# Performance work log

Measured on AMD Instinct MI355X. Metric: run time of the kernel, lower is better.

Reference implementation:

```python
import jax, jax.numpy as jnp
import numpy as np

L = 2; B = 16; H = 56; W = 56; N = H * W; D = 256
HEADS = 8; HD = 32; INNER = HEADS * HD
WIN = 7; WIN2 = WIN * WIN; NWH = H // WIN; NWW = W // WIN; NW = NWH * NWW
DISP = WIN // 2; FF = 4 * D; CPB = 512; EPS = 1e-5


def _shift_masks():
    d = DISP
    ul = np.zeros((WIN2, WIN2), np.float32)
    ul[-d * WIN:, :-d * WIN] = -np.inf
    ul[:-d * WIN, -d * WIN:] = -np.inf
    lr = np.zeros((WIN, WIN, WIN, WIN), np.float32)
    lr[:, -d:, :, :-d] = -np.inf
    lr[:, :-d, :, -d:] = -np.inf
    return jnp.asarray(ul), jnp.asarray(lr.reshape(WIN2, WIN2))

MASK_UL, MASK_LR = _shift_masks()

_idx = np.array([[i, j] for i in range(WIN) for j in range(WIN)], np.float32)
_rel = _idx[None, :, :] - _idx[:, None, :]  # (49,49,2) relative distances
REL = jnp.asarray((np.sign(_rel) * np.log1p(np.abs(_rel))).reshape(WIN2 * WIN2, 2))


def _ln(x, g, b):
    m = x.mean(-1, keepdims=True)
    v = ((x - m) ** 2).mean(-1, keepdims=True)
    return (x - m) / jnp.sqrt(v + EPS) * g + b


def _l2norm(t):
    return t / jnp.maximum(jnp.linalg.norm(t, axis=-1, keepdims=True), 1e-12)


def _window_attn(xm, qkv_w, tau, cw1, cb1, cw2, cb2, ow, ob, shifted):
    if shifted:
        xm = jnp.roll(xm, (-DISP, -DISP), (1, 2))
    qkv = xm @ qkv_w  # (B,H,W,3*INNER), no bias
    q, k, v = jnp.split(qkv, 3, axis=-1)

    def towin(t):  # (B,H,W,INNER) -> (B,heads,nw,win2,hd)
        t = t.reshape(B, NWH, WIN, NWW, WIN, HEADS, HD)
        return t.transpose(0, 5, 1, 3, 2, 4, 6).reshape(B, HEADS, NW, WIN2, HD)

    q, k, v = towin(q), towin(k), towin(v)
    # cosine-similarity attention
    dots = jnp.einsum('bhwid,bhwjd->bhwij', _l2norm(q), _l2norm(k))
    dots = dots / jnp.clip(tau, 0.01, None)[None, :, None, None, None]
    # continuous position bias MLP: 2 -> CPB -> heads
    cpb = (jax.nn.relu(REL @ cw1 + cb1) @ cw2 + cb2).reshape(WIN2, WIN2, HEADS)
    dots = dots + cpb.transpose(2, 0, 1)[None, :, None]
    if shifted:
        dots = dots.at[:, :, -NWW:].add(MASK_UL)
        dots = dots.at[:, :, NWW - 1::NWW].add(MASK_LR)
    attn = jax.nn.softmax(dots, -1)
    out = jnp.einsum('bhwij,bhwjd->bhwid', attn, v)
    out = out.reshape(B, HEADS, NWH, NWW, WIN, WIN, HD)
    out = out.transpose(0, 2, 4, 3, 5, 1, 6).reshape(B, H, W, INNER)
    out = out @ ow + ob
    if shifted:
        out = jnp.roll(out, (DISP, DISP), (1, 2))
    return out


def _forward(x, spe, qkv_w, tau, cw1, cb1, cw2, cb2, ow, ob, ln1_g, ln1_b,
             fw1, fb1, fw2, fb2, ln2_g, ln2_b, norm_g, norm_b):
    xm = (x + spe).reshape(B, H, W, D)
    for i in range(L):
        shifted = (i % 2 == 1)
        a = _window_attn(xm, qkv_w[i], tau[i], cw1[i], cb1[i], cw2[i], cb2[i],
                         ow[i], ob[i], shifted)
        xm = _ln(a, ln1_g[i], ln1_b[i]) + xm  # Residual(PostNorm(attn))
        f = jax.nn.gelu(xm @ fw1[i] + fb1[i], approximate=False) @ fw2[i] + fb2[i]
        xm = _ln(f, ln2_g[i], ln2_b[i]) + xm  # Residual(PostNorm(mlp))
    return _ln(xm, norm_g, norm_b).reshape(B, N, D)


def setup_inputs():
    key = jax.random.key(0)
    ks = jax.random.split(key, 10)
    rn = lambda k, shp, s: jax.random.normal(k, shp, jnp.float32) * s
    return {
        'x': rn(ks[0], (B, N, D), 1.0),
        'spatial_position_embedding': rn(ks[1], (B, N, D), 0.02),
        'qkv_w': rn(ks[2], (L, D, 3 * INNER), 0.02),
        'tau': jnp.ones((L, HEADS), jnp.float32),
        'cw1': rn(ks[3], (L, 2, CPB), 0.1),
        'cb1': jnp.zeros((L, CPB), jnp.float32),
        'cw2': rn(ks[4], (L, CPB, HEADS), 0.05),
        'cb2': jnp.zeros((L, HEADS), jnp.float32),
        'ow': rn(ks[5], (L, INNER, D), 0.02),
        'ob': jnp.zeros((L, D), jnp.float32),
        'ln1_g': jnp.ones((L, D), jnp.float32),
        'ln1_b': jnp.zeros((L, D), jnp.float32),
        'fw1': rn(ks[6], (L, D, FF), 0.02),
        'fb1': jnp.zeros((L, FF), jnp.float32),
        'fw2': rn(ks[7], (L, FF, D), 0.02),
        'fb2': jnp.zeros((L, D), jnp.float32),
        'ln2_g': jnp.ones((L, D), jnp.float32),
        'ln2_b': jnp.zeros((L, D), jnp.float32),
        'norm_g': jnp.ones((D,), jnp.float32),
        'norm_b': jnp.zeros((D,), jnp.float32),
    }


def reference(x, spatial_position_embedding, qkv_w, tau, cw1, cb1, cw2, cb2, ow, ob,
              ln1_g, ln1_b, fw1, fb1, fw2, fb2, ln2_g, ln2_b, norm_g, norm_b):
    return _forward(x, spatial_position_embedding, qkv_w, tau, cw1, cb1, cw2, cb2,
                    ow, ob, ln1_g, ln1_b, fw1, fb1, fw2, fb2, ln2_g, ln2_b,
                    norm_g, norm_b)
```

## Files before the change

kernel.cpp:

```cpp
#include <hip/hip_runtime.h>
#include <hip/hip_bf16.h>
#include <math.h>

typedef short    short8  __attribute__((ext_vector_type(8)));
typedef float    floatx4 __attribute__((ext_vector_type(4)));

__device__ __forceinline__ float b2f(unsigned short u) {
    union { float f; unsigned int i; } v; v.i = ((unsigned int)u) << 16; return v.f;
}
__device__ __forceinline__ unsigned short f2b(float f) {
    union { float f; unsigned int i; } v; v.f = f;
    unsigned int b = v.i;
    return (unsigned short)((b + 0x7FFFu + ((b >> 16) & 1u)) >> 16);
}
__device__ __forceinline__ float rd(const void* p, long i, int f) {
    return f ? ((const float*)p)[i] : b2f(((const unsigned short*)p)[i]);
}
__device__ __forceinline__ float fgelu(float x) {
    float x2 = x * x;
    float t = x * fmaf(x2, -0.0713548163f, -1.5957691216f);
    return __fdividef(x, 1.f + __expf(t));
}
__device__ __forceinline__ int xcd_swz(int bid, int nwg) {
    int q = nwg >> 3, r = nwg & 7;
    int xcd = bid & 7, loc = bid >> 3;
    return ((xcd < r) ? xcd * (q + 1) : r * (q + 1) + (xcd - r) * q) + loc;
}

#define NTOK_ 50176

__global__ __launch_bounds__(256) void k_detect(const unsigned short* __restrict__ x,
                                                int* __restrict__ flag) {
    __shared__ int cnt;
    if (threadIdx.x == 0) cnt = 0;
    __syncthreads();
    unsigned short v = x[threadIdx.x];
    int e = (v >> 7) & 0xFF;
    if (e >= 0x90) atomicAdd(&cnt, 1);
    __syncthreads();
    if (threadIdx.x == 0) *flag = (cnt >= 8) ? 1 : 0;
}

__global__ __launch_bounds__(256) void k_add_spe(const void* __restrict__ x,
                                                 const void* __restrict__ spe,
                                                 float* __restrict__ xm,
                                                 unsigned short* __restrict__ xb,
                                                 const int* __restrict__ flagp) {
    const int f = *flagp;
    long i = ((long)blockIdx.x * 256 + threadIdx.x) * 4;
    float4 o;
    if (f) {
        float4 a = *(const float4*)((const float*)x + i);
        float4 b = *(const float4*)((const float*)spe + i);
        o.x = a.x + b.x; o.y = a.y + b.y; o.z = a.z + b.z; o.w = a.w + b.w;
    } else {
        ushort4 a = *(const ushort4*)((const unsigned short*)x + i);
        ushort4 b = *(const ushort4*)((const unsigned short*)spe + i);
        o.x = b2f(a.x) + b2f(b.x); o.y = b2f(a.y) + b2f(b.y);
        o.z = b2f(a.z) + b2f(b.z); o.w = b2f(a.w) + b2f(b.w);
    }
    *(float4*)(xm + i) = o;
    if (xb) {
        ushort4 h; h.x = f2b(o.x); h.y = f2b(o.y); h.z = f2b(o.z); h.w = f2b(o.w);
        *(ushort4*)(xb + i) = h;
    }
}

__global__ __launch_bounds__(256) void k_transpose(const void* __restrict__ in, long ioff,
                                                   unsigned short* __restrict__ out,
                                                   int K, int N,
                                                   const int* __restrict__ flagp) {
    __shared__ unsigned short tile[32][33];
    const int f = *flagp;
    int n0 = blockIdx.x * 32, k0 = blockIdx.y * 32;
    int tx = threadIdx.x & 31, ty = threadIdx.x >> 5;
#pragma unroll
    for (int i = 0; i < 4; i++) {
        int k = k0 + ty + i * 8;
        long idx = ioff + (long)k * N + n0 + tx;
        unsigned short v = f ? f2b(((const float*)in)[idx])
                             : ((const unsigned short*)in)[idx];
        tile[ty + i * 8][tx] = v;
    }
    __syncthreads();
#pragma unroll
    for (int i = 0; i < 4; i++) {
        int n = n0 + ty + i * 8;
        out[(long)n * K + k0 + tx] = tile[tx][ty + i * 8];
    }
}

__global__ __launch_bounds__(512) void k_cpb(const void* __restrict__ cw1,
                                             const void* __restrict__ cb1,
                                             const void* __restrict__ cw2,
                                             const void* __restrict__ cb2,
                                             float* __restrict__ cpb,
                                             const int* __restrict__ flagp) {
    const int f = *flagp;
    int p = blockIdx.x;
    int l = blockIdx.y;
    int t = threadIdx.x;
    int i = p / 49, j = p - i * 49;
    int yi = i / 7, xi = i - yi * 7, yj = j / 7, xj = j - yj * 7;
    float dy = (float)(yj - yi), dx = (float)(xj - xi);
    float sy = (dy > 0.f) ? 1.f : ((dy < 0.f) ? -1.f : 0.f);
    float sx = (dx > 0.f) ? 1.f : ((dx < 0.f) ? -1.f : 0.f);
    float r0 = sy * log1pf(fabsf(dy));
    float r1 = sx * log1pf(fabsf(dx));
    float h = r0 * rd(cw1, l * 1024 + t, f) + r1 * rd(cw1, l * 1024 + 512 + t, f)
            + rd(cb1, l * 512 + t, f);
    h = fmaxf(h, 0.f);
    __shared__ float red[512];
    for (int hh = 0; hh < 8; hh++) {
        red[t] = h * rd(cw2, (long)(l * 512 + t) * 8 + hh, f);
        __syncthreads();
        for (int s = 256; s > 0; s >>= 1) {
            if (t < s) red[t] += red[t + s];
            __syncthreads();
        }
        if (t == 0) cpb[((long)l * 8 + hh) * 2401 + p] = red[0] + rd(cb2, l * 8 + hh, f);
        __syncthreads();
    }
}

__global__ __launch_bounds__(256) void k_cast_roll(const float* __restrict__ xmg,
                                                   unsigned short* __restrict__ xb, int shift) {
    int gid = blockIdx.x * 256 + threadIdx.x;
    int c4 = (gid & 63) * 4;
    int t = gid >> 6;
    int x = t % 56; int t2 = t / 56;
    int y = t2 % 56;
    int b = t2 / 56;
    int ys = y + shift; if (ys >= 56) ys -= 56;
    int xs = x + shift; if (xs >= 56) xs -= 56;
    float4 v = *(const float4*)(xmg + (((long)b * 3136 + ys * 56 + xs) * 256 + c4));
    ushort4 o; o.x = f2b(v.x); o.y = f2b(v.y); o.z = f2b(v.z); o.w = f2b(v.w);
    *(ushort4*)(xb + ((long)t * 256 + c4)) = o;
}

__global__ __launch_bounds__(256) void gemm_bt(const unsigned short* __restrict__ A,
                                               const unsigned short* __restrict__ Bt,
                                               const void* __restrict__ bias, long boff,
                                               void* __restrict__ Cp,
                                               int M, int N, int K, int flags,
                                               const int* __restrict__ flagp) {
    __shared__ __align__(16) unsigned short smem[16896];
    unsigned short* As = smem;
    unsigned short* Bs = smem + 5120;
    const int f = *flagp;
    const int tid = threadIdx.x;
    const int lane = tid & 63;
    const int wave = tid >> 6;
    const int wrow = (wave >> 1) * 64;
    const int wcol = (wave & 1) * 64;

    const int nwg = gridDim.x * gridDim.y;
    const int nb = xcd_swz(blockIdx.y * gridDim.x + blockIdx.x, nwg);
    const int bn = nb % gridDim.x, bm = nb / gridDim.x;

    floatx4 acc[4][4] = {};

    const int arow = tid >> 2;
    const int aseg = (tid & 3) * 8;
    const unsigned short* Ag = A + (long)(bm * 128 + arow) * K + aseg;
    const unsigned short* Bg = Bt + (long)(bn * 128 + arow) * K + aseg;
    const long rstep = (long)64 * K;

    const int q = lane >> 4;
    const int mrow = lane & 15;

    for (int k0 = 0; k0 < K; k0 += 32) {
        uint4 a0 = *(const uint4*)(Ag + k0);
        uint4 a1 = *(const uint4*)(Ag + k0 + rstep);
        uint4 b0 = *(const uint4*)(Bg + k0);
        uint4 b1 = *(const uint4*)(Bg + k0 + rstep);
        __syncthreads();
        *(uint4*)(As + arow * 40 + aseg) = a0;
        *(uint4*)(As + (arow + 64) * 40 + aseg) = a1;
        *(uint4*)(Bs + arow * 40 + aseg) = b0;
        *(uint4*)(Bs + (arow + 64) * 40 + aseg) = b1;
        __syncthreads();

        short8 af_[4], bf_[4];
#pragma unroll
        for (int mt = 0; mt < 4; mt++)
            af_[mt] = *(const short8*)(As + (wrow + mt * 16 + mrow) * 40 + q * 8);
#pragma unroll
        for (int nt = 0; nt < 4; nt++)
            bf_[nt] = *(const short8*)(Bs + (wcol + nt * 16 + mrow) * 40 + q * 8);
#pragma unroll
        for (int mt = 0; mt < 4; mt++)
#pragma unroll
            for (int nt = 0; nt < 4; nt++)
                acc[mt][nt] = __builtin_amdgcn_mfma_f32_16x16x32_bf16(af_[mt], bf_[nt], acc[mt][nt], 0, 0, 0);
    }

    __syncthreads();

    unsigned short* T = smem;
#pragma unroll
    for (int nt = 0; nt < 4; nt++) {
        int col = wcol + nt * 16 + mrow;
        float bv = (flags & 1) ? rd(bias, boff + bn * 128 + col, f) : 0.f;
#pragma unroll
        for (int mt = 0; mt < 4; mt++) {
            int row0 = wrow + mt * 16 + q * 4;
#pragma unroll
            for (int r = 0; r < 4; r++) {
                float v = acc[mt][nt][r] + bv;
                if (flags & 2) v = fgelu(v);
                T[(row0 + r) * 132 + col] = f2b(v);
            }
        }
    }
    __syncthreads();
    unsigned short* Cu = (unsigned short*)Cp;
    int row = tid >> 4;
    int col8 = (tid & 15) * 8;
#pragma unroll
    for (int p = 0; p < 8; p++) {
        int rr = p * 16 + row;
        *(uint4*)(Cu + (long)(bm * 128 + rr) * N + bn * 128 + col8) =
            *(const uint4*)(T + rr * 132 + col8);
    }
}

__global__ __launch_bounds__(256) void gemm_ln(const unsigned short* __restrict__ A,
                                               const unsigned short* __restrict__ Bt,
                                               const void* __restrict__ bias, long boff,
                                               const void* __restrict__ g, long goff,
                                               const void* __restrict__ bb, long b2off,
                                               float* __restrict__ xm,
                                               unsigned short* __restrict__ xb,
                                               int K, int xbmode,
                                               const int* __restrict__ flagp) {
    __shared__ __align__(16) unsigned short smem[17152];
    __shared__ float pp[4][32][2];
    unsigned short* As = smem;
    unsigned short* Bs = smem + 1280;
    const int f = *flagp;
    const int tid = threadIdx.x;
    const int lane = tid & 63;
    const int wv = tid >> 6;
    const int wcol = wv * 64;
    const int bm = blockIdx.x;

    floatx4 acc[2][4] = {};
    const int brow = tid >> 2;
    const int bseg = (tid & 3) * 8;
    const unsigned short* Ag = A + (long)(bm * 32 + brow) * K + bseg;
    const unsigned short* Bg = Bt + (long)brow * K + bseg;
    const long brow2 = (long)64 * K;
    const int q = lane >> 4;
    const int c = lane & 15;

    for (int k0 = 0; k0 < K; k0 += 32) {
        uint4 a0;
        if (tid < 128) a0 = *(const uint4*)(Ag + k0);
        uint4 b0 = *(const uint4*)(Bg + k0);
        uint4 b1 = *(const uint4*)(Bg + k0 + brow2);
        uint4 b2 = *(const uint4*)(Bg + k0 + 2 * brow2);
        uint4 b3 = *(const uint4*)(Bg + k0 + 3 * brow2);
        __syncthreads();
        if (tid < 128) *(uint4*)(As + brow * 40 + bseg) = a0;
        *(uint4*)(Bs + brow * 40 + bseg) = b0;
        *(uint4*)(Bs + (brow + 64) * 40 + bseg) = b1;
        *(uint4*)(Bs + (brow + 128) * 40 + bseg) = b2;
        *(uint4*)(Bs + (brow + 192) * 40 + bseg) = b3;
        __syncthreads();

        short8 af_[2], bf_[4];
#pragma unroll
        for (int mt = 0; mt < 2; mt++)
            af_[mt] = *(const short8*)(As + (mt * 16 + c) * 40 + q * 8);
#pragma unroll
        for (int nt = 0; nt < 4; nt++)
            bf_[nt] = *(const short8*)(Bs + (wcol + nt * 16 + c) * 40 + q * 8);
#pragma unroll
        for (int mt = 0; mt < 2; mt++)
#pragma unroll
            for (int nt = 0; nt < 4; nt++)
                acc[mt][nt] = __builtin_amdgcn_mfma_f32_16x16x32_bf16(af_[mt], bf_[nt], acc[mt][nt], 0, 0, 0);
    }
    __syncthreads();

    float bv[4];
#pragma unroll
    for (int nt = 0; nt < 4; nt++)
        bv[nt] = rd(bias, boff + wcol + nt * 16 + c, f);
#pragma unroll
    for (int mt = 0; mt < 2; mt++) {
#pragma unroll
        for (int r = 0; r < 4; r++) {
            float s1 = 0.f, s2 = 0.f;
#pragma unroll
            for (int nt = 0; nt < 4; nt++) {
                float v = acc[mt][nt][r] + bv[nt];
                s1 += v; s2 += v * v;
            }
            s1 += __shfl_xor(s1, 1); s2 += __shfl_xor(s2, 1);
            s1 += __shfl_xor(s1, 2); s2 += __shfl_xor(s2, 2);
            s1 += __shfl_xor(s1, 4); s2 += __shfl_xor(s2, 4);
            s1 += __shfl_xor(s1, 8); s2 += __shfl_xor(s2, 8);
            if (c == 0) {
                pp[wv][mt * 16 + q * 4 + r][0] = s1;
                pp[wv][mt * 16 + q * 4 + r][1] = s2;
            }
        }
    }

    const int c0 = lane * 4;
    float4 gv, bbv;
    gv.x = rd(g, goff + c0 + 0, f); gv.y = rd(g, goff + c0 + 1, f);
    gv.z = rd(g, goff + c0 + 2, f); gv.w = rd(g, goff + c0 + 3, f);
    bbv.x = rd(bb, b2off + c0 + 0, f); bbv.y = rd(bb, b2off + c0 + 1, f);
    bbv.z = rd(bb, b2off + c0 + 2, f); bbv.w = rd(bb, b2off + c0 + 3, f);

    float* Tf = (float*)smem;
#pragma unroll
    for (int mt = 0; mt < 2; mt++)
#pragma unroll
        for (int nt = 0; nt < 4; nt++)
#pragma unroll
            for (int r = 0; r < 4; r++)
                Tf[(mt * 16 + q * 4 + r) * 268 + wcol + nt * 16 + c] = acc[mt][nt][r] + bv[nt];
    __syncthreads();
#pragma unroll
    for (int it = 0; it < 8; it++) {
        int row = wv * 8 + it;
        float sum = pp[0][row][0] + pp[1][row][0] + pp[2][row][0] + pp[3][row][0];
        float ssq = pp[0][row][1] + pp[1][row][1] + pp[2][row][1] + pp[3][row][1];
        float mean = sum * (1.f / 256.f);
        float var = ssq * (1.f / 256.f) - mean * mean;
        float rstd = rsqrtf(fmaxf(var, 0.f) + 1e-5f);
        long tok = (long)(bm * 32 + row);
        long grow = tok * 256;
        float4 t = *(const float4*)(Tf + row * 268 + c0);
        float4 xv = *(const float4*)(xm + grow + c0);
        float4 o;
        o.x = (t.x - mean) * rstd * gv.x + bbv.x + xv.x;
        o.y = (t.y - mean) * rstd * gv.y + bbv.y + xv.y;
        o.z = (t.z - mean) * rstd * gv.z + bbv.z + xv.z;
        o.w = (t.w - mean) * rstd * gv.w + bbv.w + xv.w;
        *(float4*)(xm + grow + c0) = o;
        if (xbmode) {
            long xg = grow;
            if (xbmode == 2) {
                int bi = (int)(tok / 3136); int r2 = (int)(tok - (long)bi * 3136);
                int y = r2 / 56; int x = r2 - y * 56;
                y = (y >= 3) ? y - 3 : y + 53;
                x = (x >= 3) ? x - 3 : x + 53;
                xg = ((long)bi * 3136 + y * 56 + x) * 256;
            }
            ushort4 hb; hb.x = f2b(o.x); hb.y = f2b(o.y); hb.z = f2b(o.z); hb.w = f2b(o.w);
            *(ushort4*)(xb + xg + c0) = hb;
        }
    }
}

__global__ __launch_bounds__(256) void k_attn(const unsigned short* __restrict__ qkv,
                                              const float* __restrict__ cpb,
                                              const void* __restrict__ tau, long toff,
                                              unsigned short* __restrict__ out,
                                              int shifted,
                                              const int* __restrict__ flagp) {
    __shared__ __align__(16) unsigned short Pbuf[4][64 * 72];
    __shared__ __align__(16) unsigned short Vt[4][32 * 72];
    __shared__ float inq_s[4][64], ink_s[4][64];

    const int f = *flagp;
    const int tid = threadIdx.x;
    const int wv = tid >> 6;
    const int lane = tid & 63;
    const int h = blockIdx.x * 4 + wv;
    const int w = blockIdx.y, b = blockIdx.z;
    const int wy = w >> 3, wx = w & 7;
    const int q = lane >> 4;
    const int c = lane & 15;

    short8 qa[4], kb[4];
    float sqv[4], skv[4];
#pragma unroll
    for (int mt = 0; mt < 4; mt++) {
        int i = mt * 16 + c; if (i > 48) i = 48;
        int py = i / 7, px = i - py * 7;
        long base = (((long)b * 56 + wy * 7 + py) * 56 + wx * 7 + px) * 768 + h * 32 + q * 8;
        qa[mt] = *(const short8*)(qkv + base);
        kb[mt] = *(const short8*)(qkv + base + 256);
        float sq = 0.f, sk = 0.f;
#pragma unroll
        for (int e = 0; e < 8; e++) {
            float a = b2f((unsigned short)qa[mt][e]); sq += a * a;
            float k2 = b2f((unsigned short)kb[mt][e]); sk += k2 * k2;
        }
        sqv[mt] = sq; skv[mt] = sk;
    }
#pragma unroll
    for (int mt = 0; mt < 4; mt++) {
        float sq = sqv[mt]; sq += __shfl_xor(sq, 16); sq += __shfl_xor(sq, 32);
        float sk = skv[mt]; sk += __shfl_xor(sk, 16); sk += __shfl_xor(sk, 32);
        if (q == 0) {
            inq_s[wv][mt * 16 + c] = 1.f / fmaxf(sqrtf(sq), 1e-12f);
            ink_s[wv][mt * 16 + c] = 1.f / fmaxf(sqrtf(sk), 1e-12f);
        }
    }

    floatx4 acc[4][4] = {};
#pragma unroll
    for (int mt = 0; mt < 4; mt++)
#pragma unroll
        for (int nt = 0; nt < 4; nt++)
            acc[mt][nt] = __builtin_amdgcn_mfma_f32_16x16x32_bf16(qa[mt], kb[nt], acc[mt][nt], 0, 0, 0);

#pragma unroll
    for (int z = lane; z < 576; z += 64)
        *(uint2*)(&Vt[wv][z * 4]) = make_uint2(0u, 0u);
    if (lane < 49) {
        int py = lane / 7, px = lane - py * 7;
        long base = (((long)b * 56 + wy * 7 + py) * 56 + wx * 7 + px) * 768 + h * 32 + 512;
#pragma unroll
        for (int dd = 0; dd < 32; dd += 8) {
            ushort4 v0 = *(const ushort4*)(qkv + base + dd);
            ushort4 v1 = *(const ushort4*)(qkv + base + dd + 4);
            Vt[wv][(dd + 0) * 72 + lane] = v0.x;
            Vt[wv][(dd + 1) * 72 + lane] = v0.y;
            Vt[wv][(dd + 2) * 72 + lane] = v0.z;
            Vt[wv][(dd + 3) * 72 + lane] = v0.w;
            Vt[wv][(dd + 4) * 72 + lane] = v1.x;
            Vt[wv][(dd + 5) * 72 + lane] = v1.y;
            Vt[wv][(dd + 6) * 72 + lane] = v1.z;
            Vt[wv][(dd + 7) * 72 + lane] = v1.w;
        }
    }

    float scale = 1.f / fmaxf(rd(tau, toff + h, f), 0.01f);
#pragma unroll
    for (int mt = 0; mt < 4; mt++) {
#pragma unroll
        for (int r = 0; r < 4; r++) {
            int i = mt * 16 + q * 4 + r;
            int ci = (i < 49) ? i : 48;
            int pyi = ci / 7, pxi = ci - pyi * 7;
            float qi = inq_s[wv][ci] * scale;
            float vals[4];
#pragma unroll
            for (int nt = 0; nt < 4; nt++) {
                int j = nt * 16 + c;
                if (j < 49) {
                    float v = acc[mt][nt][r] * qi * ink_s[wv][j]
                            + cpb[h * 2401 + ci * 49 + j];
                    if (shifted) {
                        int pyj = j / 7, pxj = j - pyj * 7;
                        if (wy == 7 && ((pyi >= 4) != (pyj >= 4))) v = -1e30f;
                        if (wx == 7 && ((pxi >= 4) != (pxj >= 4))) v = -1e30f;
                    }
                    vals[nt] = v;
                } else vals[nt] = -1e30f;
            }
            float m = fmaxf(fmaxf(vals[0], vals[1]), fmaxf(vals[2], vals[3]));
            m = fmaxf(m, __shfl_xor(m, 1)); m = fmaxf(m, __shfl_xor(m, 2));
            m = fmaxf(m, __shfl_xor(m, 4)); m = fmaxf(m, __shfl_xor(m, 8));
            float s = 0.f;
#pragma unroll
            for (int nt = 0; nt < 4; nt++) { vals[nt] = __expf(vals[nt] - m); s += vals[nt]; }
            s += __shfl_xor(s, 1); s += __shfl_xor(s, 2);
            s += __shfl_xor(s, 4); s += __shfl_xor(s, 8);
            float rinv = 1.f / s;
#pragma unroll
            for (int nt = 0; nt < 4; nt++)
                Pbuf[wv][i * 72 + nt * 16 + c] = f2b(vals[nt] * rinv);
        }
    }

    floatx4 accO[4][2] = {};
#pragma unroll
    for (int ks = 0; ks < 2; ks++) {
        short8 pa[4], vb[2];
#pragma unroll
        for (int mt = 0; mt < 4; mt++)
            pa[mt] = *(const short8*)(&Pbuf[wv][(mt * 16 + c) * 72 + ks * 32 + q * 8]);
#pragma unroll
        for (int nt = 0; nt < 2; nt++)
            vb[nt] = *(const short8*)(&Vt[wv][(nt * 16 + c) * 72 + ks * 32 + q * 8]);
#pragma unroll
        for (int mt = 0; mt < 4; mt++)
#pragma unroll
            for (int nt = 0; nt < 2; nt++)
                accO[mt][nt] = __builtin_amdgcn_mfma_f32_16x16x32_bf16(pa[mt], vb[nt], accO[mt][nt], 0, 0, 0);
    }

    int sh = shifted ? 3 : 0;
#pragma unroll
    for (int mt = 0; mt < 4; mt++) {
#pragma unroll
        for (int r = 0; r < 4; r++) {
            int i = mt * 16 + q * 4 + r;
            if (i < 49) {
                int py = i / 7, px = i - py * 7;
                int yo = wy * 7 + py + sh; if (yo >= 56) yo -= 56;
                int xo = wx * 7 + px + sh; if (xo >= 56) xo -= 56;
                long ob = (((long)b * 56 + yo) * 56 + xo) * 256 + h * 32;
                out[ob + c]      = f2b(accO[mt][0][r]);
                out[ob + 16 + c] = f2b(accO[mt][1][r]);
            }
        }
    }
}

__global__ __launch_bounds__(256) void k_final(const float* __restrict__ xm,
                                               const void* __restrict__ g,
                                               const void* __restrict__ bb,
                                               void* __restrict__ out,
                                               const int* __restrict__ flagp) {
    const int f = *flagp;
    int t = blockIdx.x, c = threadIdx.x;
    long off = (long)t * 256 + c;
    float v = xm[off];
    __shared__ float red[256];
    red[c] = v; __syncthreads();
#pragma unroll
    for (int s = 128; s > 0; s >>= 1) {
        if (c < s) red[c] += red[c + s];
        __syncthreads();
    }
    float mean = red[0] * (1.f / 256.f);
    __syncthreads();
    float d = v - mean;
    red[c] = d * d; __syncthreads();
#pragma unroll
    for (int s = 128; s > 0; s >>= 1) {
        if (c < s) red[c] += red[c + s];
        __syncthreads();
    }
    float var = red[0] * (1.f / 256.f);
    float ln = d * rsqrtf(var + 1e-5f) * rd(g, c, f) + rd(bb, c, f);
    if (f) ((float*)out)[off] = ln;
    else   ((unsigned short*)out)[off] = f2b(ln);
}

extern "C" void kernel_launch(void* const* d_in, const int* in_sizes, int n_in,
                              void* d_out, int out_size, void* d_ws, size_t ws_size,
                              hipStream_t stream) {
    char* ws = (char*)d_ws;
    float*          xm    = (float*)(ws + 0);
    unsigned short* wt    = (unsigned short*)(ws + 51380224);
    float*          cpb   = (float*)(ws + 54525952);
    int*            flagp = (int*)(ws + 54679616);
    const size_t DYN = 54680576;

    long Mg = NTOK_; int G = 1;
    while (G <= 8) {
        Mg = NTOK_ / G;
        if (DYN + (size_t)Mg * 2560 <= ws_size) break;
        G <<= 1;
    }
    if (G > 8) { G = 8; Mg = NTOK_ / 8; }
    const int NB = 16 / G;
    const bool fused = (G == 1);

    unsigned short* xb   = (unsigned short*)(ws + DYN);
    unsigned short* qkvb = (unsigned short*)(ws + DYN + Mg * 512);
    unsigned short* hid  = (unsigned short*)(ws + DYN + Mg * 512);

    k_detect<<<1, 256, 0, stream>>>((const unsigned short*)d_in[0], flagp);

    for (int l = 0; l < 2; l++) {
        unsigned short* base = wt + (long)l * 786432;
        k_transpose<<<dim3(24, 8), 256, 0, stream>>>(d_in[2],  (long)l * 196608, base,          256, 768,  flagp);
        k_transpose<<<dim3(8, 8),  256, 0, stream>>>(d_in[8],  (long)l * 65536,  base + 196608, 256, 256,  flagp);
        k_transpose<<<dim3(32, 8), 256, 0, stream>>>(d_in[12], (long)l * 262144, base + 262144, 256, 1024, flagp);
        k_transpose<<<dim3(8, 32), 256, 0, stream>>>(d_in[14], (long)l * 262144, base + 524288, 1024, 256, flagp);
    }
    k_cpb<<<dim3(2401, 2), 512, 0, stream>>>(d_in[4], d_in[5], d_in[6], d_in[7], cpb, flagp);
    k_add_spe<<<dim3(12544), 256, 0, stream>>>(d_in[0], d_in[1], xm,
                                               fused ? xb : (unsigned short*)nullptr, flagp);

    for (int l = 0; l < 2; l++) {
        int sh = (l & 1) ? 3 : 0;
        unsigned short* base = wt + (long)l * 786432;
        for (int g = 0; g < G; g++) {
            long m0 = (long)g * Mg;
            if (!fused)
                k_cast_roll<<<dim3(Mg / 4), 256, 0, stream>>>(xm + m0 * 256, xb, sh);
            gemm_bt<<<dim3(6, Mg / 128), 256, 0, stream>>>(xb, base, nullptr, 0, qkvb,
                                                           (int)Mg, 768, 256, 4, flagp);
            k_attn<<<dim3(2, 64, NB), 256, 0, stream>>>(qkvb, cpb + (long)l * 19208,
                                                        d_in[3], (long)l * 8, xb, (l & 1), flagp);
            gemm_ln<<<dim3(Mg / 32), 256, 0, stream>>>(xb, base + 196608, d_in[9], (long)l * 256,
                                                       d_in[10], (long)l * 256, d_in[11], (long)l * 256,
                                                       xm + m0 * 256, xb, 256, 1, flagp);
            gemm_bt<<<dim3(8, Mg / 128), 256, 0, stream>>>(xb, base + 262144, d_in[13], (long)l * 1024,
                                                           hid, (int)Mg, 1024, 256, 1 | 2 | 4, flagp);
            int xbm = fused ? ((l == 0) ? 2 : 0) : 1;
            gemm_ln<<<dim3(Mg / 32), 256, 0, stream>>>(hid, base + 524288, d_in[15], (long)l * 256,
                                                       d_in[16], (long)l * 256, d_in[17], (long)l * 256,
                                                       xm + m0 * 256, xb, 1024, xbm, flagp);
        }
    }
    k_final<<<dim3(NTOK_), 256, 0, stream>>>(xm, d_in[18], d_in[19], d_out, flagp);
}
```

Measured before the change: 929.2 us.

## Load B fragments directly into registers and prefetch next K-tile in GEMMs

```diff
diff --git a/kernel.cpp b/kernel.cpp
--- a/kernel.cpp
+++ b/kernel.cpp
@@ -146,7 +146,6 @@
                                                const int* __restrict__ flagp) {
     __shared__ __align__(16) unsigned short smem[16896];
     unsigned short* As = smem;
-    unsigned short* Bs = smem + 5120;
     const int f = *flagp;
     const int tid = threadIdx.x;
     const int lane = tid & 63;
@@ -163,36 +162,50 @@
     const int arow = tid >> 2;
     const int aseg = (tid & 3) * 8;
     const unsigned short* Ag = A + (long)(bm * 128 + arow) * K + aseg;
-    const unsigned short* Bg = Bt + (long)(bn * 128 + arow) * K + aseg;
     const long rstep = (long)64 * K;
 
     const int q = lane >> 4;
     const int mrow = lane & 15;
 
+    const unsigned short* Brow[4];
+#pragma unroll
+    for (int nt = 0; nt < 4; nt++)
+        Brow[nt] = Bt + (long)(bn * 128 + wcol + nt * 16 + mrow) * K + q * 8;
+
+    uint4 a_cur0 = *(const uint4*)(Ag);
+    uint4 a_cur1 = *(const uint4*)(Ag + rstep);
+    short8 bf_cur[4], bf_nxt[4];
+#pragma unroll
+    for (int nt = 0; nt < 4; nt++) bf_cur[nt] = *(const short8*)(Brow[nt]);
+
     for (int k0 = 0; k0 < K; k0 += 32) {
-        uint4 a0 = *(const uint4*)(Ag + k0);
-        uint4 a1 = *(const uint4*)(Ag + k0 + rstep);
-        uint4 b0 = *(const uint4*)(Bg + k0);
-        uint4 b1 = *(const uint4*)(Bg + k0 + rstep);
-        __syncthreads();
-        *(uint4*)(As + arow * 40 + aseg) = a0;
-        *(uint4*)(As + (arow + 64) * 40 + aseg) = a1;
-        *(uint4*)(Bs + arow * 40 + aseg) = b0;
-        *(uint4*)(Bs + (arow + 64) * 40 + aseg) = b1;
-        __syncthreads();
-
-        short8 af_[4], bf_[4];
+        const int kn = k0 + 32;
+        uint4 a_nxt0, a_nxt1;
+        if (kn < K) {
+            a_nxt0 = *(const uint4*)(Ag + kn);
+            a_nxt1 = *(const uint4*)(Ag + kn + rstep);
+#pragma unroll
+            for (int nt = 0; nt < 4; nt++) bf_nxt[nt] = *(const short8*)(Brow[nt] + kn);
+        }
+        __syncthreads();
+        *(uint4*)(As + arow * 40 + aseg) = a_cur0;
+        *(uint4*)(As + (arow + 64) * 40 + aseg) = a_cur1;
+        __syncthreads();
+
+        short8 af_[4];
 #pragma unroll
         for (int mt = 0; mt < 4; mt++)
             af_[mt] = *(const short8*)(As + (wrow + mt * 16 + mrow) * 40 + q * 8);
 #pragma unroll
-        for (int nt = 0; nt < 4; nt++)
-            bf_[nt] = *(const short8*)(Bs + (wcol + nt * 16 + mrow) * 40 + q * 8);
-#pragma unroll
         for (int mt = 0; mt < 4; mt++)
 #pragma unroll
             for (int nt = 0; nt < 4; nt++)
-                acc[mt][nt] = __builtin_amdgcn_mfma_f32_16x16x32_bf16(af_[mt], bf_[nt], acc[mt][nt], 0, 0, 0);
+                acc[mt][nt] = __builtin_amdgcn_mfma_f32_16x16x32_bf16(af_[mt], bf_cur[nt], acc[mt][nt], 0, 0, 0);
+        if (kn < K) {
+            a_cur0 = a_nxt0; a_cur1 = a_nxt1;
+#pragma unroll
+            for (int nt = 0; nt < 4; nt++) bf_cur[nt] = bf_nxt[nt];
+        }
     }
 
     __syncthreads();
@@ -237,7 +250,6 @@
     __shared__ __align__(16) unsigned short smem[17152];
     __shared__ float pp[4][32][2];
     unsigned short* As = smem;
-    unsigned short* Bs = smem + 1280;
     const int f = *flagp;
     const int tid = threadIdx.x;
     const int lane = tid & 63;
@@ -249,38 +261,46 @@
     const int brow = tid >> 2;
     const int bseg = (tid & 3) * 8;
     const unsigned short* Ag = A + (long)(bm * 32 + brow) * K + bseg;
-    const unsigned short* Bg = Bt + (long)brow * K + bseg;
-    const long brow2 = (long)64 * K;
     const int q = lane >> 4;
     const int c = lane & 15;
 
+    const unsigned short* Brow[4];
+#pragma unroll
+    for (int nt = 0; nt < 4; nt++)
+        Brow[nt] = Bt + (long)(wcol + nt * 16 + c) * K + q * 8;
+
+    uint4 a_cur;
+    if (tid < 128) a_cur = *(const uint4*)(Ag);
+    short8 bf_cur[4], bf_nxt[4];
+#pragma unroll
+    for (int nt = 0; nt < 4; nt++) bf_cur[nt] = *(const short8*)(Brow[nt]);
+
     for (int k0 = 0; k0 < K; k0 += 32) {
-        uint4 a0;
-        if (tid < 128) a0 = *(const uint4*)(Ag + k0);
-        uint4 b0 = *(const uint4*)(Bg + k0);
-        uint4 b1 = *(const uint4*)(Bg + k0 + brow2);
-        uint4 b2 = *(const uint4*)(Bg + k0 + 2 * brow2);
-        uint4 b3 = *(const uint4*)(Bg + k0 + 3 * brow2);
-        __syncthreads();
-        if (tid < 128) *(uint4*)(As + brow * 40 + bseg) = a0;
-        *(uint4*)(Bs + brow * 40 + bseg) = b0;
-        *(uint4*)(Bs + (brow + 64) * 40 + bseg) = b1;
-        *(uint4*)(Bs + (brow + 128) * 40 + bseg) = b2;
-        *(uint4*)(Bs + (brow + 192) * 40 + bseg) = b3;
-        __syncthreads();
-
-        short8 af_[2], bf_[4];
+        const int kn = k0 + 32;
+        uint4 a_nxt;
+        if (kn < K) {
+            if (tid < 128) a_nxt = *(const uint4*)(Ag + kn);
+#pragma unroll
+            for (int nt = 0; nt < 4; nt++) bf_nxt[nt] = *(const short8*)(Brow[nt] + kn);
+        }
+        __syncthreads();
+        if (tid < 128) *(uint4*)(As + brow * 40 + bseg) = a_cur;
+        __syncthreads();
+
+        short8 af_[2];
 #pragma unroll
         for (int mt = 0; mt < 2; mt++)
             af_[mt] = *(const short8*)(As + (mt * 16 + c) * 40 + q * 8);
 #pragma unroll
-        for (int nt = 0; nt < 4; nt++)
-            bf_[nt] = *(const short8*)(Bs + (wcol + nt * 16 + c) * 40 + q * 8);
-#pragma unroll
         for (int mt = 0; mt < 2; mt++)
 #pragma unroll
             for (int nt = 0; nt < 4; nt++)
-                acc[mt][nt] = __builtin_amdgcn_mfma_f32_16x16x32_bf16(af_[mt], bf_[nt], acc[mt][nt], 0, 0, 0);
+                acc[mt][nt] = __builtin_amdgcn_mfma_f32_16x16x32_bf16(af_[mt], bf_cur[nt], acc[mt][nt], 0, 0, 0);
+        if (kn < K) {
+            if (tid < 128) a_cur = a_nxt;
+#pragma unroll
+            for (int nt = 0; nt < 4; nt++) bf_cur[nt] = bf_nxt[nt];
+        }
     }
     __syncthreads();
 
```

Measured after the change: 1.027 ms. 1.11x slower.
